# Kernel tuning notes

Measured on AMD Instinct MI355X. Metric: run time of the kernel, lower is better.

The kernel has to match this reference:

```python
import jax, jax.numpy as jnp
import numpy as np

# ---- config (matches init_kwargs) ----
SPATIAL_SCALE = 0.0625
POOLED = 7
OUT_DIM = 256
SAMPLE_PER_PART = 4
TRANS_STD = 0.1
PART_SIZE = 7
DEFORM_FC_DIM = 1024
# group_size == 1 -> position-sensitive group index is always 0, channel c == ctop


def _deform_roi_pool(feat, rois, offset, no_trans):
    """Faithful JAX port of DeformablePSROIPoolForward (DCNv2), group_size=1.
    feat: (B,C,H,W), rois: (N,5)=[b,x1,y1,x2,y2], offset: (N,2,P,P) or None.
    Returns (N,C,P,P)."""
    B, C, H, W = feat.shape
    N = rois.shape[0]
    P, S = POOLED, SAMPLE_PER_PART
    dt = feat.dtype
    featT = jnp.transpose(feat, (0, 2, 3, 1))  # (B,H,W,C) for spatial gathers

    b = rois[:, 0].astype(jnp.int32)
    rsw = jnp.round(rois[:, 1]) * SPATIAL_SCALE - 0.5
    rsh = jnp.round(rois[:, 2]) * SPATIAL_SCALE - 0.5
    rew = (jnp.round(rois[:, 3]) + 1.0) * SPATIAL_SCALE - 0.5
    reh = (jnp.round(rois[:, 4]) + 1.0) * SPATIAL_SCALE - 0.5
    roi_w = jnp.maximum(rew - rsw, 0.1)
    roi_h = jnp.maximum(reh - rsh, 0.1)
    bin_h = roi_h / P            # (N,)
    bin_w = roi_w / P
    sub_h = bin_h / S
    sub_w = bin_w / S

    ph = jnp.arange(P)
    pw = jnp.arange(P)
    part_h = jnp.floor(ph.astype(dt) / P * PART_SIZE).astype(jnp.int32)  # == ph when part_size==P
    part_w = jnp.floor(pw.astype(dt) / P * PART_SIZE).astype(jnp.int32)

    if no_trans:
        tx = jnp.zeros((N, P, P), dt)
        ty = jnp.zeros((N, P, P), dt)
    else:
        tx = offset[:, 0][:, part_h][:, :, part_w] * TRANS_STD  # (N,P,P)
        ty = offset[:, 1][:, part_h][:, :, part_w] * TRANS_STD

    hstart = ph.astype(dt)[None, :, None] * bin_h[:, None, None] + rsh[:, None, None] + ty * roi_h[:, None, None]
    wstart = pw.astype(dt)[None, None, :] * bin_w[:, None, None] + rsw[:, None, None] + tx * roi_w[:, None, None]

    ih = jnp.arange(S).astype(dt)
    iw = jnp.arange(S).astype(dt)
    # sample coords, shape (N,P,P,S,S); ih along axis -2, iw along axis -1
    h = hstart[..., None, None] + ih[:, None] * sub_h[:, None, None, None, None]
    w = wstart[..., None, None] + iw[None, :] * sub_w[:, None, None, None, None]

    valid = (w >= -0.5) & (w <= W - 0.5) & (h >= -0.5) & (h <= H - 0.5)
    hc = jnp.clip(h, 0.0, H - 1.0)
    wc = jnp.clip(w, 0.0, W - 1.0)
    h0 = jnp.floor(hc).astype(jnp.int32)
    w0 = jnp.floor(wc).astype(jnp.int32)
    h1 = jnp.minimum(h0 + 1, H - 1)
    w1 = jnp.minimum(w0 + 1, W - 1)
    lh = hc - h0.astype(dt)
    lw = wc - w0.astype(dt)

    bidx = b[:, None, None, None, None]

    def g(yy, xx):  # (N,P,P,S,S,C)
        return featT[bidx, yy, xx]

    val = (g(h0, w0) * ((1 - lh) * (1 - lw))[..., None]
           + g(h0, w1) * ((1 - lh) * lw)[..., None]
           + g(h1, w0) * (lh * (1 - lw))[..., None]
           + g(h1, w1) * (lh * lw)[..., None])
    val = jnp.where(valid[..., None], val, jnp.zeros((), dt))
    ssum = val.sum(axis=(3, 4))                       # (N,P,P,C)
    cnt = valid.sum(axis=(3, 4)).astype(dt)           # (N,P,P)
    out = jnp.where(cnt[..., None] > 0, ssum / jnp.maximum(cnt, 1.0)[..., None], jnp.zeros((), dt))
    return jnp.transpose(out, (0, 3, 1, 2))           # (N,C,P,P)


def setup_inputs() -> dict:
    key = jax.random.key(0)
    ks = jax.random.split(key, 12)
    B, C, H, W = 2, OUT_DIM, 100, 100
    N = 512
    img = H / SPATIAL_SCALE  # 1600

    feat = jax.random.normal(ks[0], (B, C, H, W), jnp.float32)

    bi = jax.random.randint(ks[1], (N,), 0, B).astype(jnp.float32)
    x1 = jax.random.uniform(ks[2], (N,), jnp.float32, 0.0, img - 420.0)
    y1 = jax.random.uniform(ks[3], (N,), jnp.float32, 0.0, img - 420.0)
    x2 = x1 + jax.random.uniform(ks[4], (N,), jnp.float32, 32.0, 400.0)
    y2 = y1 + jax.random.uniform(ks[5], (N,), jnp.float32, 32.0, 400.0)
    rois = jnp.stack([bi, x1, y1, x2, y2], axis=1)

    fin = POOLED * POOLED * OUT_DIM  # 12544
    w1 = jax.random.normal(ks[6], (DEFORM_FC_DIM, fin), jnp.float32) / np.sqrt(fin)
    b1 = jnp.zeros((DEFORM_FC_DIM,), jnp.float32)
    w2 = jax.random.normal(ks[7], (DEFORM_FC_DIM, DEFORM_FC_DIM), jnp.float32) / np.sqrt(DEFORM_FC_DIM)
    b2 = jnp.zeros((DEFORM_FC_DIM,), jnp.float32)
    # original init zeroes the last layer; use small random so offsets/mask are non-trivial
    w3 = jax.random.normal(ks[8], (POOLED * POOLED * 3, DEFORM_FC_DIM), jnp.float32) * 0.01
    b3 = jnp.zeros((POOLED * POOLED * 3,), jnp.float32)
    return {"input": feat, "rois": rois, "w1": w1, "b1": b1, "w2": w2, "b2": b2, "w3": w3, "b3": b3}


def reference(input, rois, w1, b1, w2, b2, w3, b3):
    N = rois.shape[0]
    P = POOLED
    # pass 1: plain (no_trans) deformable RoI pooling to predict offsets/mask
    roi0 = _deform_roi_pool(input, rois, None, no_trans=True)      # (N,C,P,P)
    x = roi0.reshape(N, -1)
    x = jax.nn.relu(x @ w1.T + b1)
    x = jax.nn.relu(x @ w2.T + b2)
    om = (x @ w3.T + b3).reshape(N, 3, P, P)
    offset = om[:, 0:2]                                            # (N,2,P,P) [trans_x, trans_y]
    mask = jax.nn.sigmoid(om[:, 2:3])                              # (N,1,P,P)
    # pass 2: deformable pooling with learned offsets, modulated by mask
    out = _deform_roi_pool(input, rois, offset, no_trans=False) * mask
    return out
```

## Files before the change

kernel.cpp:

```cpp
#include <hip/hip_runtime.h>

#define BB 2
#define CC 256
#define HH 100
#define WW 100
#define NROI 512
#define KDIM 12544
#define FC 1024

typedef _Float16 half_t;
typedef _Float16 f16x2 __attribute__((ext_vector_type(2)));
typedef _Float16 f16x8 __attribute__((ext_vector_type(8)));
typedef _Float16 f16x4 __attribute__((ext_vector_type(4)));
typedef float f32x4 __attribute__((ext_vector_type(4)));

__device__ __forceinline__ void gload16(const half_t* g, half_t* l) {
  __builtin_amdgcn_global_load_lds(
      (const __attribute__((address_space(1))) unsigned int*)g,
      (__attribute__((address_space(3))) unsigned int*)l, 16, 0, 0);
}

__global__ __launch_bounds__(256) void prep(const float* __restrict__ feat,
                                            half_t* __restrict__ featT,
                                            const float* __restrict__ w1,
                                            half_t* __restrict__ w1h,
                                            const float* __restrict__ w2,
                                            half_t* __restrict__ w2h) {
  int bid = blockIdx.x;
  if (bid < 12544) {
    int i4 = (bid * 256 + threadIdx.x) * 4;
    float4 v = *(const float4*)(w1 + i4);
    f16x4 o;
    o[0] = (half_t)v.x; o[1] = (half_t)v.y; o[2] = (half_t)v.z; o[3] = (half_t)v.w;
    *(f16x4*)(w1h + i4) = o;
    return;
  }
  bid -= 12544;
  if (bid < 1024) {
    int i4 = (bid * 256 + threadIdx.x) * 4;
    float4 v = *(const float4*)(w2 + i4);
    f16x4 o;
    o[0] = (half_t)v.x; o[1] = (half_t)v.y; o[2] = (half_t)v.z; o[3] = (half_t)v.w;
    *(f16x4*)(w2h + i4) = o;
    return;
  }
  bid -= 1024;
  __shared__ float tile[32][33];
  const int bx = bid % 313;
  const int rem = bid / 313;
  const int by = rem & 7;
  const int bz = rem >> 3;
  const int tx = threadIdx.x & 31, ty = threadIdx.x >> 5;
  const int hw0 = bx * 32;
  const int c0 = by * 32;
  const float* fb = feat + (size_t)bz * CC * (HH * WW);
#pragma unroll
  for (int i = 0; i < 4; i++) {
    int c = c0 + ty + i * 8;
    int hw = hw0 + tx;
    tile[ty + i * 8][tx] = (hw < HH * WW) ? fb[(size_t)c * (HH * WW) + hw] : 0.0f;
  }
  __syncthreads();
  half_t* ob = featT + (size_t)bz * (HH * WW) * CC;
#pragma unroll
  for (int i = 0; i < 4; i++) {
    int hw = hw0 + ty + i * 8;
    int c = c0 + tx;
    if (hw < HH * WW) ob[(size_t)hw * CC + c] = (half_t)tile[tx][ty + i * 8];
  }
}

struct PixW { int idx; float w; };

template <bool PASS2>
__global__ __launch_bounds__(512) void pool_kernel(const half_t* __restrict__ featT,
                                                   const float* __restrict__ rois,
                                                   const float* __restrict__ part3,
                                                   const float* __restrict__ b3,
                                                   half_t* __restrict__ xout,
                                                   float* __restrict__ out) {
  __shared__ __align__(16) PixW s_pix[49 * 32];
  __shared__ int s_cnt[49];
  __shared__ float s_scale[49];
  __shared__ float  s_outf[PASS2 ? KDIM : 1];
  __shared__ half_t s_outh[PASS2 ? 1 : KDIM];

  const int n = blockIdx.x;
  const int tid = threadIdx.x;
  const float* r = rois + n * 5;
  const int b = (int)r[0];
  const float rsw = rintf(r[1]) * 0.0625f - 0.5f;
  const float rsh = rintf(r[2]) * 0.0625f - 0.5f;
  const float rew = (rintf(r[3]) + 1.0f) * 0.0625f - 0.5f;
  const float reh = (rintf(r[4]) + 1.0f) * 0.0625f - 0.5f;
  const float roi_w = fmaxf(rew - rsw, 0.1f);
  const float roi_h = fmaxf(reh - rsh, 0.1f);
  const float bin_h = roi_h / 7.0f, bin_w = roi_w / 7.0f;
  const float sub_h = bin_h * 0.25f, sub_w = bin_w * 0.25f;
  const half_t* fb = featT + (size_t)b * (HH * WW) * CC;

  if (tid < 49) {
    const int p = tid, ph = p / 7, pw = p - ph * 7;
    float tx = 0.0f, ty = 0.0f, mask = 1.0f;
    if (PASS2) {
      float o0 = b3[p], o1 = b3[49 + p], o2 = b3[98 + p];
#pragma unroll
      for (int zz = 0; zz < 8; zz++) {
        const float* pz = part3 + ((size_t)zz * NROI + n) * 147;
        o0 += pz[p]; o1 += pz[49 + p]; o2 += pz[98 + p];
      }
      tx = o0 * 0.1f;
      ty = o1 * 0.1f;
      mask = 1.0f / (1.0f + expf(-o2));
    }
    const float hst = (float)ph * bin_h + rsh + ty * roi_h;
    const float wst = (float)pw * bin_w + rsw + tx * roi_w;
    float wh[6] = {0, 0, 0, 0, 0, 0};
    float hc0 = fminf(fmaxf(hst, 0.0f), 99.0f);
    const int r0 = (int)hc0;
    int rtop = r0;
    float vsh = 0.0f;
#pragma unroll
    for (int i = 0; i < 4; i++) {
      float h = hst + (float)i * sub_h;
      bool v = (h >= -0.5f) && (h <= (float)HH - 0.5f);
      float hc = fminf(fmaxf(h, 0.0f), 99.0f);
      int h0 = (int)hc;
      float lh = hc - (float)h0;
      int h1 = min(h0 + 1, HH - 1);
      if (v) { wh[h0 - r0] += 1.0f - lh; wh[h1 - r0] += lh; vsh += 1.0f; }
      rtop = h1;
    }
    float wwc[6] = {0, 0, 0, 0, 0, 0};
    float wc0 = fminf(fmaxf(wst, 0.0f), 99.0f);
    const int c0 = (int)wc0;
    int ctop = c0;
    float vsw = 0.0f;
#pragma unroll
    for (int j = 0; j < 4; j++) {
      float w = wst + (float)j * sub_w;
      bool v = (w >= -0.5f) && (w <= (float)WW - 0.5f);
      float wc = fminf(fmaxf(w, 0.0f), 99.0f);
      int w0 = (int)wc;
      float lw = wc - (float)w0;
      int w1 = min(w0 + 1, WW - 1);
      if (v) { wwc[w0 - c0] += 1.0f - lw; wwc[w1 - c0] += lw; vsw += 1.0f; }
      ctop = w1;
    }
    const int nr = rtop - r0 + 1, nc = ctop - c0 + 1;
    float cntf = vsh * vsw;
    s_scale[p] = (cntf > 0.0f) ? mask / cntf : 0.0f;
    PixW* dst = &s_pix[p * 32];
    int m = 0;
    for (int ri = 0; ri < nr; ri++) {
      int rowoff = (r0 + ri) * WW + c0;
      for (int ci = 0; ci < nc; ci++) {
        dst[m].idx = (rowoff + ci) * CC;
        dst[m].w = wh[ri] * wwc[ci];
        m++;
      }
    }
    while (m & 7) { dst[m].idx = 0; dst[m].w = 0.0f; m++; }
    s_cnt[p] = m;
  }
  __syncthreads();

  const int wv = tid >> 6;
  const int c4 = (tid & 63) * 4;
  for (int p = wv; p < 49; p += 8) {
    const int cnt = __builtin_amdgcn_readfirstlane(s_cnt[p]);
    const PixW* cp = &s_pix[p * 32];
    float a0 = 0.0f, a1 = 0.0f, a2 = 0.0f, a3 = 0.0f;
    for (int q = 0; q < cnt; q += 8) {
      const uint4* cp4 = (const uint4*)(cp + q);
      uint4 e0 = cp4[0], e1 = cp4[1], e2 = cp4[2], e3 = cp4[3];
      int i0 = __builtin_amdgcn_readfirstlane(e0.x);
      float sw0 = __uint_as_float(__builtin_amdgcn_readfirstlane(e0.y));
      int i1 = __builtin_amdgcn_readfirstlane(e0.z);
      float sw1 = __uint_as_float(__builtin_amdgcn_readfirstlane(e0.w));
      int i2 = __builtin_amdgcn_readfirstlane(e1.x);
      float sw2 = __uint_as_float(__builtin_amdgcn_readfirstlane(e1.y));
      int i3 = __builtin_amdgcn_readfirstlane(e1.z);
      float sw3 = __uint_as_float(__builtin_amdgcn_readfirstlane(e1.w));
      int i4_ = __builtin_amdgcn_readfirstlane(e2.x);
      float sw4 = __uint_as_float(__builtin_amdgcn_readfirstlane(e2.y));
      int i5 = __builtin_amdgcn_readfirstlane(e2.z);
      float sw5 = __uint_as_float(__builtin_amdgcn_readfirstlane(e2.w));
      int i6 = __builtin_amdgcn_readfirstlane(e3.x);
      float sw6 = __uint_as_float(__builtin_amdgcn_readfirstlane(e3.y));
      int i7 = __builtin_amdgcn_readfirstlane(e3.z);
      float sw7 = __uint_as_float(__builtin_amdgcn_readfirstlane(e3.w));
      f16x4 v0 = *(const f16x4*)(fb + i0 + c4);
      f16x4 v1 = *(const f16x4*)(fb + i1 + c4);
      f16x4 v2 = *(const f16x4*)(fb + i2 + c4);
      f16x4 v3 = *(const f16x4*)(fb + i3 + c4);
      f16x4 v4 = *(const f16x4*)(fb + i4_ + c4);
      f16x4 v5 = *(const f16x4*)(fb + i5 + c4);
      f16x4 v6 = *(const f16x4*)(fb + i6 + c4);
      f16x4 v7 = *(const f16x4*)(fb + i7 + c4);
      a0 += sw0 * (float)v0[0] + sw1 * (float)v1[0] + sw2 * (float)v2[0] + sw3 * (float)v3[0]
          + sw4 * (float)v4[0] + sw5 * (float)v5[0] + sw6 * (float)v6[0] + sw7 * (float)v7[0];
      a1 += sw0 * (float)v0[1] + sw1 * (float)v1[1] + sw2 * (float)v2[1] + sw3 * (float)v3[1]
          + sw4 * (float)v4[1] + sw5 * (float)v5[1] + sw6 * (float)v6[1] + sw7 * (float)v7[1];
      a2 += sw0 * (float)v0[2] + sw1 * (float)v1[2] + sw2 * (float)v2[2] + sw3 * (float)v3[2]
          + sw4 * (float)v4[2] + sw5 * (float)v5[2] + sw6 * (float)v6[2] + sw7 * (float)v7[2];
      a3 += sw0 * (float)v0[3] + sw1 * (float)v1[3] + sw2 * (float)v2[3] + sw3 * (float)v3[3]
          + sw4 * (float)v4[3] + sw5 * (float)v5[3] + sw6 * (float)v6[3] + sw7 * (float)v7[3];
    }
    float sc = s_scale[p];
    a0 *= sc; a1 *= sc; a2 *= sc; a3 *= sc;
    if (PASS2) {
      s_outf[(c4 + 0) * 49 + p] = a0;
      s_outf[(c4 + 1) * 49 + p] = a1;
      s_outf[(c4 + 2) * 49 + p] = a2;
      s_outf[(c4 + 3) * 49 + p] = a3;
    } else {
      s_outh[(c4 + 0) * 49 + p] = (half_t)a0;
      s_outh[(c4 + 1) * 49 + p] = (half_t)a1;
      s_outh[(c4 + 2) * 49 + p] = (half_t)a2;
      s_outh[(c4 + 3) * 49 + p] = (half_t)a3;
    }
  }
  __syncthreads();

  if (PASS2) {
    float* ob = out + (size_t)n * KDIM;
    for (int l = tid * 4; l < KDIM; l += 2048)
      *(float4*)(ob + l) = *(const float4*)(s_outf + l);
  } else {
    half_t* ob = xout + (size_t)n * KDIM;
    for (int l = tid * 8; l < KDIM; l += 4096)
      *(f16x8*)(ob + l) = *(const f16x8*)(s_outh + l);
  }
}

template <int SK>
__global__ __launch_bounds__(256, 2) void gemm_lds(const half_t* __restrict__ A,
                                                   const half_t* __restrict__ B,
                                                   float* __restrict__ P, int K) {
  __shared__ half_t As[2][128 * 64];
  __shared__ half_t Bs[2][128 * 64];
  const int d = blockIdx.x + gridDim.x * (blockIdx.y + gridDim.y * blockIdx.z);
  const int g = (d & 7) * (SK * 4) + (d >> 3);
  const int z = g >> 5;
  const int tile = g & 31;
  const int m0 = (tile & 3) * 128;
  const int n0 = (tile >> 2) * 128;
  const int Kc = K / SK;
  const int kbeg = z * Kc;
  const int tid = threadIdx.x;
  const int lane = tid & 63;
  const int wave = tid >> 6;
  const int wm = (wave & 1) * 64;
  const int wn = (wave >> 1) * 64;
  const int fr = lane & 15;
  const int kc0 = lane >> 4;
  const int lr = lane >> 3;
  const int lc = (lane & 7) ^ lr;
  const half_t* Ag = A + (size_t)(m0 + wave * 8 + lr) * K + kbeg + lc * 8;
  const half_t* Bg = B + (size_t)(n0 + wave * 8 + lr) * K + kbeg + lc * 8;
  f32x4 acc[4][4] = {};

  auto stage = [&](int buf, int ko) {
#pragma unroll
    for (int s = 0; s < 4; s++)
      gload16(Ag + (size_t)(32 * s) * K + ko, &As[buf][s * 2048 + wave * 512]);
#pragma unroll
    for (int s = 0; s < 4; s++)
      gload16(Bg + (size_t)(32 * s) * K + ko, &Bs[buf][s * 2048 + wave * 512]);
  };

  const int iters = Kc >> 6;
  stage(0, 0);
  if (iters > 1) {
    stage(1, 64);
    asm volatile("s_waitcnt vmcnt(8)" ::: "memory");
  } else {
    asm volatile("s_waitcnt vmcnt(0)" ::: "memory");
  }
  __builtin_amdgcn_s_barrier();

  for (int it = 0; it < iters; it++) {
    const int cur = it & 1;
#pragma unroll
    for (int ks = 0; ks < 2; ks++) {
      const int swz = ((kc0 + ks * 4) ^ (fr & 7)) * 8;
      f16x8 af[4], bf[4];
#pragma unroll
      for (int i = 0; i < 4; i++) af[i] = *(const f16x8*)&As[cur][(wm + i * 16 + fr) * 64 + swz];
#pragma unroll
      for (int j = 0; j < 4; j++) bf[j] = *(const f16x8*)&Bs[cur][(wn + j * 16 + fr) * 64 + swz];
#pragma unroll
      for (int i = 0; i < 4; i++)
#pragma unroll
        for (int j = 0; j < 4; j++)
          acc[i][j] = __builtin_amdgcn_mfma_f32_16x16x32_f16(af[i], bf[j], acc[i][j], 0, 0, 0);
    }
    asm volatile("s_waitcnt lgkmcnt(0)" ::: "memory");
    __builtin_amdgcn_s_barrier();
    const bool issue = (it + 2 < iters);
    if (issue) stage(cur, (it + 2) * 64);
    if (it + 1 < iters) {
      if (issue) asm volatile("s_waitcnt vmcnt(8)" ::: "memory");
      else       asm volatile("s_waitcnt vmcnt(0)" ::: "memory");
      __builtin_amdgcn_s_barrier();
    }
  }
  float* Pz = P + (((size_t)z * 32 + tile) * 4 + wave) * 4096;
#pragma unroll
  for (int i = 0; i < 4; i++)
#pragma unroll
    for (int j = 0; j < 4; j++)
#pragma unroll
      for (int rr = 0; rr < 4; rr++)
        Pz[((i * 4 + j) * 4 + rr) * 64 + lane] = acc[i][j][rr];
}

template <bool OUT16, bool RELU, int SK>
__global__ __launch_bounds__(256) void reduce_blocked(const float* __restrict__ P,
                                                      const float* __restrict__ bias,
                                                      void* __restrict__ out,
                                                      int MN, int N) {
  int i4 = (blockIdx.x * 256 + threadIdx.x) * 4;
  if (i4 >= MN) return;
  float4 s = *(const float4*)(P + i4);
#pragma unroll
  for (int z = 1; z < SK; z++) {
    float4 t = *(const float4*)(P + (size_t)z * MN + i4);
    s.x += t.x; s.y += t.y; s.z += t.z; s.w += t.w;
  }
  const int lane0 = i4 & 63;
  const int q     = (i4 >> 6) & 63;
  const int wave  = (i4 >> 12) & 3;
  const int bx    = (i4 >> 14) & 3;
  const int by    = (i4 >> 16) & 7;
  const int rr = q & 3, j_ = (q >> 2) & 3, i_ = q >> 4;
  const int row = bx * 128 + (wave & 1) * 64 + i_ * 16 + (lane0 >> 4) * 4 + rr;
  const int col = by * 128 + (wave >> 1) * 64 + j_ * 16 + (lane0 & 15);
  float4 bv = *(const float4*)(bias + col);
  s.x += bv.x; s.y += bv.y; s.z += bv.z; s.w += bv.w;
  if (RELU) {
    s.x = fmaxf(s.x, 0.0f); s.y = fmaxf(s.y, 0.0f);
    s.z = fmaxf(s.z, 0.0f); s.w = fmaxf(s.w, 0.0f);
  }
  size_t o = (size_t)row * N + col;
  if (OUT16) {
    f16x4 ov;
    ov[0] = (half_t)s.x; ov[1] = (half_t)s.y; ov[2] = (half_t)s.z; ov[3] = (half_t)s.w;
    *(f16x4*)((half_t*)out + o) = ov;
  } else {
    *(float4*)((float*)out + o) = s;
  }
}

__global__ __launch_bounds__(192) void gemm3_part(const float* __restrict__ h2,
                                                  const float* __restrict__ w3,
                                                  float* __restrict__ part3) {
  __shared__ float hs[8][128];
  const int n0 = blockIdx.x * 8;
  const int z = blockIdx.y;
  const int tid = threadIdx.x;
  for (int idx = tid; idx < 1024; idx += 192) {
    int nn = idx >> 7, kk = idx & 127;
    hs[nn][kk] = h2[(size_t)(n0 + nn) * FC + z * 128 + kk];
  }
  __syncthreads();
  const int j = tid;
  if (j < 147) {
    const float* wr = w3 + (size_t)j * FC + z * 128;
    float acc[8] = {0, 0, 0, 0, 0, 0, 0, 0};
    for (int k = 0; k < 128; k += 4) {
      float4 wv = *(const float4*)(wr + k);
#pragma unroll
      for (int nn = 0; nn < 8; nn++)
        acc[nn] += hs[nn][k] * wv.x + hs[nn][k + 1] * wv.y +
                   hs[nn][k + 2] * wv.z + hs[nn][k + 3] * wv.w;
    }
#pragma unroll
    for (int nn = 0; nn < 8; nn++)
      part3[((size_t)z * NROI + n0 + nn) * 147 + j] = acc[nn];
  }
}

extern "C" void kernel_launch(void* const* d_in, const int* in_sizes, int n_in,
                              void* d_out, int out_size, void* d_ws, size_t ws_size,
                              hipStream_t stream) {
  const float* feat = (const float*)d_in[0];
  const float* rois = (const float*)d_in[1];
  const float* w1 = (const float*)d_in[2];
  const float* b1 = (const float*)d_in[3];
  const float* w2 = (const float*)d_in[4];
  const float* b2 = (const float*)d_in[5];
  const float* w3 = (const float*)d_in[6];
  const float* b3 = (const float*)d_in[7];
  float* out = (float*)d_out;
  char* ws = (char*)d_ws;

  half_t* featT = (half_t*)ws;
  half_t* xh    = (half_t*)(ws + 10240000);
  half_t* w1h   = (half_t*)(ws + 23085056);
  half_t* w2h   = (half_t*)(ws + 48775168);
  half_t* h1    = (half_t*)(ws + 50872320);
  float*  h2    = (float*)(ws + 51920896);
  float*  part  = (float*)(ws + 54319104);

  const int MN = NROI * FC;

  prep<<<dim3(18576), dim3(256), 0, stream>>>(feat, featT, w1, w1h, w2, w2h);
  pool_kernel<false><<<dim3(NROI), dim3(512), 0, stream>>>(featT, rois, nullptr, nullptr, xh, nullptr);

  gemm_lds<14><<<dim3(4, 8, 14), dim3(256), 0, stream>>>(xh, w1h, part, KDIM);
  reduce_blocked<true, true, 14><<<dim3(MN / 1024), dim3(256), 0, stream>>>(part, b1, (void*)h1, MN, FC);

  gemm_lds<8><<<dim3(4, 8, 8), dim3(256), 0, stream>>>(h1, w2h, part, FC);
  reduce_blocked<false, true, 8><<<dim3(MN / 1024), dim3(256), 0, stream>>>(part, b2, (void*)h2, MN, FC);

  gemm3_part<<<dim3(64, 8), dim3(192), 0, stream>>>(h2, w3, part);
  pool_kernel<true><<<dim3(NROI), dim3(512), 0, stream>>>(featT, rois, part, b3, nullptr, out);
}
```

Measured before the change: 225.8 us.

## Gather 8 channels per lane with half-wave pixel split; raise MFMA priority

The pooling gather now has each lane load 8 fp16 channels (16-byte loads) instead of 4. The two half-waves each process alternate pixel-weight entries and are combined with a cross-lane xor-32 shuffle before scaling and the LDS store. This halves the number of pixel iterations per half-wave and widens each load. In exchange it adds shuffles and idles half the lanes during the store. Separately, the GEMM raises wave priority around its MFMA block with s_setprio to favour matrix issue over other waves.

```diff
diff --git a/kernel.cpp b/kernel.cpp
--- a/kernel.cpp
+++ b/kernel.cpp
@@ -166,59 +166,57 @@
   __syncthreads();
 
   const int wv = tid >> 6;
-  const int c4 = (tid & 63) * 4;
+  const int lane = tid & 63;
+  const int half = lane >> 5;
+  const int c8 = (lane & 31) * 8;
   for (int p = wv; p < 49; p += 8) {
-    const int cnt = __builtin_amdgcn_readfirstlane(s_cnt[p]);
+    const int cnt = s_cnt[p];
     const PixW* cp = &s_pix[p * 32];
-    float a0 = 0.0f, a1 = 0.0f, a2 = 0.0f, a3 = 0.0f;
+    float a0 = 0, a1 = 0, a2 = 0, a3 = 0, a4 = 0, a5 = 0, a6 = 0, a7 = 0;
     for (int q = 0; q < cnt; q += 8) {
-      const uint4* cp4 = (const uint4*)(cp + q);
-      uint4 e0 = cp4[0], e1 = cp4[1], e2 = cp4[2], e3 = cp4[3];
-      int i0 = __builtin_amdgcn_readfirstlane(e0.x);
-      float sw0 = __uint_as_float(__builtin_amdgcn_readfirstlane(e0.y));
-      int i1 = __builtin_amdgcn_readfirstlane(e0.z);
-      float sw1 = __uint_as_float(__builtin_amdgcn_readfirstlane(e0.w));
-      int i2 = __builtin_amdgcn_readfirstlane(e1.x);
-      float sw2 = __uint_as_float(__builtin_amdgcn_readfirstlane(e1.y));
-      int i3 = __builtin_amdgcn_readfirstlane(e1.z);
-      float sw3 = __uint_as_float(__builtin_amdgcn_readfirstlane(e1.w));
-      int i4_ = __builtin_amdgcn_readfirstlane(e2.x);
-      float sw4 = __uint_as_float(__builtin_amdgcn_readfirstlane(e2.y));
-      int i5 = __builtin_amdgcn_readfirstlane(e2.z);
-      float sw5 = __uint_as_float(__builtin_amdgcn_readfirstlane(e2.w));
-      int i6 = __builtin_amdgcn_readfirstlane(e3.x);
-      float sw6 = __uint_as_float(__builtin_amdgcn_readfirstlane(e3.y));
-      int i7 = __builtin_amdgcn_readfirstlane(e3.z);
-      float sw7 = __uint_as_float(__builtin_amdgcn_readfirstlane(e3.w));
-      f16x4 v0 = *(const f16x4*)(fb + i0 + c4);
-      f16x4 v1 = *(const f16x4*)(fb + i1 + c4);
-      f16x4 v2 = *(const f16x4*)(fb + i2 + c4);
-      f16x4 v3 = *(const f16x4*)(fb + i3 + c4);
-      f16x4 v4 = *(const f16x4*)(fb + i4_ + c4);
-      f16x4 v5 = *(const f16x4*)(fb + i5 + c4);
-      f16x4 v6 = *(const f16x4*)(fb + i6 + c4);
-      f16x4 v7 = *(const f16x4*)(fb + i7 + c4);
-      a0 += sw0 * (float)v0[0] + sw1 * (float)v1[0] + sw2 * (float)v2[0] + sw3 * (float)v3[0]
-          + sw4 * (float)v4[0] + sw5 * (float)v5[0] + sw6 * (float)v6[0] + sw7 * (float)v7[0];
-      a1 += sw0 * (float)v0[1] + sw1 * (float)v1[1] + sw2 * (float)v2[1] + sw3 * (float)v3[1]
-          + sw4 * (float)v4[1] + sw5 * (float)v5[1] + sw6 * (float)v6[1] + sw7 * (float)v7[1];
-      a2 += sw0 * (float)v0[2] + sw1 * (float)v1[2] + sw2 * (float)v2[2] + sw3 * (float)v3[2]
-          + sw4 * (float)v4[2] + sw5 * (float)v5[2] + sw6 * (float)v6[2] + sw7 * (float)v7[2];
-      a3 += sw0 * (float)v0[3] + sw1 * (float)v1[3] + sw2 * (float)v2[3] + sw3 * (float)v3[3]
-          + sw4 * (float)v4[3] + sw5 * (float)v5[3] + sw6 * (float)v6[3] + sw7 * (float)v7[3];
-    }
-    float sc = s_scale[p];
-    a0 *= sc; a1 *= sc; a2 *= sc; a3 *= sc;
-    if (PASS2) {
-      s_outf[(c4 + 0) * 49 + p] = a0;
-      s_outf[(c4 + 1) * 49 + p] = a1;
-      s_outf[(c4 + 2) * 49 + p] = a2;
-      s_outf[(c4 + 3) * 49 + p] = a3;
-    } else {
-      s_outh[(c4 + 0) * 49 + p] = (half_t)a0;
-      s_outh[(c4 + 1) * 49 + p] = (half_t)a1;
-      s_outh[(c4 + 2) * 49 + p] = (half_t)a2;
-      s_outh[(c4 + 3) * 49 + p] = (half_t)a3;
+      PixW e0 = cp[q + 0 + half];
+      PixW e1 = cp[q + 2 + half];
+      PixW e2 = cp[q + 4 + half];
+      PixW e3 = cp[q + 6 + half];
+      f16x8 v0 = *(const f16x8*)(fb + e0.idx + c8);
+      f16x8 v1 = *(const f16x8*)(fb + e1.idx + c8);
+      f16x8 v2 = *(const f16x8*)(fb + e2.idx + c8);
+      f16x8 v3 = *(const f16x8*)(fb + e3.idx + c8);
+      a0 += e0.w * (float)v0[0] + e1.w * (float)v1[0] + e2.w * (float)v2[0] + e3.w * (float)v3[0];
+      a1 += e0.w * (float)v0[1] + e1.w * (float)v1[1] + e2.w * (float)v2[1] + e3.w * (float)v3[1];
+      a2 += e0.w * (float)v0[2] + e1.w * (float)v1[2] + e2.w * (float)v2[2] + e3.w * (float)v3[2];
+      a3 += e0.w * (float)v0[3] + e1.w * (float)v1[3] + e2.w * (float)v2[3] + e3.w * (float)v3[3];
+      a4 += e0.w * (float)v0[4] + e1.w * (float)v1[4] + e2.w * (float)v2[4] + e3.w * (float)v3[4];
+      a5 += e0.w * (float)v0[5] + e1.w * (float)v1[5] + e2.w * (float)v2[5] + e3.w * (float)v3[5];
+      a6 += e0.w * (float)v0[6] + e1.w * (float)v1[6] + e2.w * (float)v2[6] + e3.w * (float)v3[6];
+      a7 += e0.w * (float)v0[7] + e1.w * (float)v1[7] + e2.w * (float)v2[7] + e3.w * (float)v3[7];
+    }
+    a0 += __shfl_xor(a0, 32); a1 += __shfl_xor(a1, 32);
+    a2 += __shfl_xor(a2, 32); a3 += __shfl_xor(a3, 32);
+    a4 += __shfl_xor(a4, 32); a5 += __shfl_xor(a5, 32);
+    a6 += __shfl_xor(a6, 32); a7 += __shfl_xor(a7, 32);
+    if (half == 0) {
+      float sc = s_scale[p];
+      a0 *= sc; a1 *= sc; a2 *= sc; a3 *= sc; a4 *= sc; a5 *= sc; a6 *= sc; a7 *= sc;
+      if (PASS2) {
+        s_outf[(c8 + 0) * 49 + p] = a0;
+        s_outf[(c8 + 1) * 49 + p] = a1;
+        s_outf[(c8 + 2) * 49 + p] = a2;
+        s_outf[(c8 + 3) * 49 + p] = a3;
+        s_outf[(c8 + 4) * 49 + p] = a4;
+        s_outf[(c8 + 5) * 49 + p] = a5;
+        s_outf[(c8 + 6) * 49 + p] = a6;
+        s_outf[(c8 + 7) * 49 + p] = a7;
+      } else {
+        s_outh[(c8 + 0) * 49 + p] = (half_t)a0;
+        s_outh[(c8 + 1) * 49 + p] = (half_t)a1;
+        s_outh[(c8 + 2) * 49 + p] = (half_t)a2;
+        s_outh[(c8 + 3) * 49 + p] = (half_t)a3;
+        s_outh[(c8 + 4) * 49 + p] = (half_t)a4;
+        s_outh[(c8 + 5) * 49 + p] = (half_t)a5;
+        s_outh[(c8 + 6) * 49 + p] = (half_t)a6;
+        s_outh[(c8 + 7) * 49 + p] = (half_t)a7;
+      }
     }
   }
   __syncthreads();
@@ -290,11 +288,13 @@
       for (int i = 0; i < 4; i++) af[i] = *(const f16x8*)&As[cur][(wm + i * 16 + fr) * 64 + swz];
 #pragma unroll
       for (int j = 0; j < 4; j++) bf[j] = *(const f16x8*)&Bs[cur][(wn + j * 16 + fr) * 64 + swz];
+      __builtin_amdgcn_s_setprio(1);
 #pragma unroll
       for (int i = 0; i < 4; i++)
 #pragma unroll
         for (int j = 0; j < 4; j++)
           acc[i][j] = __builtin_amdgcn_mfma_f32_16x16x32_f16(af[i], bf[j], acc[i][j], 0, 0, 0);
+      __builtin_amdgcn_s_setprio(0);
     }
     asm volatile("s_waitcnt lgkmcnt(0)" ::: "memory");
     __builtin_amdgcn_s_barrier();
```

Result: faster. 220.3 us (-2.4%).
